# Optimization experiments

Measured on AMD Instinct MI355X. Metric: run time of the kernel, lower is better.

## Reference

```python
import jax, jax.numpy as jnp
import numpy as np

EPS = 1e-4
TAU = 0.1
GAMMA = 64.0
RADIUS = 1.0
N_HEADS = 4
N_SPLIT = 4


def _l2norm(x, axis=-1):
    return x / jnp.maximum(jnp.linalg.norm(x, axis=axis, keepdims=True), 1e-12)


def _pd2(a, b):
    # pairwise squared distances: (B,N,M)
    return (jnp.sum(a * a, -1)[:, :, None] + jnp.sum(b * b, -1)[:, None, :]
            - 2.0 * jnp.einsum('bnd,bmd->bnm', a, b))


def _sim_matrix(xyz, nf, radius, gamma):
    # radius-masked Gaussian feature affinity, zero diagonal
    N = xyz.shape[1]
    d2x = _pd2(xyz, xyz)
    d2f = _pd2(nf, nf)
    A = jnp.exp(-gamma * d2f / nf.shape[-1]) * (d2x < radius * radius).astype(nf.dtype)
    return A * (1.0 - jnp.eye(N, dtype=A.dtype))


def _norm_lap(A, eps):
    deg = A.sum(-1)
    dinv = jax.lax.rsqrt(deg + eps)
    na = A * dinv[:, :, None] * dinv[:, None, :]
    lap = jnp.eye(A.shape[1], dtype=A.dtype) - na
    return lap, na


def _mincut(X, na, W1, b1, W2, b2, tau):
    # one GCN layer + temperature softmax soft assignment; pooled = weighted mean
    h = jax.nn.relu(jnp.einsum('bnm,bmc->bnc', na, X) @ W1 + b1)
    s = jax.nn.softmax((h @ W2 + b2) / tau, axis=-1)  # (B,N,K)
    denom = s.sum(1)[:, :, None] + EPS                # (B,K,1)
    c_fea = jnp.einsum('bnk,bnc->bkc', s, X) / denom
    return c_fea, s


def _centers(xyz, s):
    denom = s.sum(1)[:, :, None] + EPS
    return jnp.einsum('bnk,bnd->bkd', s, xyz) / denom


def _assignment_loss(p_xyz, c_xyz, s):
    d2 = _pd2(p_xyz, c_xyz)
    return jnp.mean(jnp.sum(s * d2, -1))


def _welsch(p_xyz, c_xyz, sigma):
    d2min = jnp.min(_pd2(p_xyz, c_xyz), -1)
    return jnp.mean(1.0 - jnp.exp(-d2min / (2.0 * sigma * sigma)))


def _knn_affinity(xyz, k):
    N = xyz.shape[1]
    d2 = _pd2(xyz, xyz)
    eye = jnp.eye(N, dtype=d2.dtype)
    neg = -(d2 + 1e6 * eye)
    thresh = jax.lax.top_k(neg, k)[0][..., -1:]
    mask = (neg >= thresh).astype(d2.dtype)
    A = jnp.exp(-d2) * mask * (1.0 - eye)
    return jnp.maximum(A, jnp.swapaxes(A, 1, 2))


def _cut_loss(na, xyz, alpha):
    N = xyz.shape[1]
    lap = jnp.eye(N, dtype=na.dtype) - na
    quad = jnp.einsum('bnd,bnm,bmd->b', xyz, lap, xyz)
    return alpha * jnp.mean(quad / N)


def _cross_attn(gf, cf, Wq, Wk, Wv, Wo, n_heads):
    B, N, C = gf.shape
    M = cf.shape[1]
    dh = C // n_heads
    q = (gf @ Wq).reshape(B, N, n_heads, dh)
    k = (cf @ Wk).reshape(B, M, n_heads, dh)
    v = (cf @ Wv).reshape(B, M, n_heads, dh)
    scores = jnp.einsum('bnhd,bmhd->bhnm', q, k) / np.sqrt(dh).astype(np.float32)
    attn = jax.nn.softmax(scores, -1)
    out = jnp.einsum('bhnm,bmhd->bnhd', attn, v).reshape(B, N, C) @ Wo
    return out, attn.mean(1)


def setup_inputs() -> dict:
    key = jax.random.key(0)
    ks = jax.random.split(key, 20)
    B, N_sp, C, H, K = 2, 1024, 256, 128, 64
    Kg = K // N_SPLIT
    sc = 1.0 / np.sqrt(C)
    sh = 1.0 / np.sqrt(H)
    return {
        'g_fea': jax.random.normal(ks[0], (B, N_sp, C), jnp.float32),
        'g_xyz': jax.random.uniform(ks[1], (B, N_sp, 3), jnp.float32),
        'p_fea_0': jax.random.normal(ks[2], (B, 4096, C), jnp.float32),
        'p_xyz_0': jax.random.uniform(ks[3], (B, 4096, 3), jnp.float32),
        'p_fea_1': jax.random.normal(ks[4], (B, 2048, C), jnp.float32),
        'p_xyz_1': jax.random.uniform(ks[5], (B, 2048, 3), jnp.float32),
        'lW1': jax.random.normal(ks[6], (C, H), jnp.float32) * sc,
        'lb1': jnp.zeros((H,), jnp.float32),
        'lW2': jax.random.normal(ks[7], (H, K), jnp.float32) * sh,
        'lb2': jnp.zeros((K,), jnp.float32),
        'gW1': jax.random.normal(ks[8], (C, H), jnp.float32) * sc,
        'gb1': jnp.zeros((H,), jnp.float32),
        'gW2': jax.random.normal(ks[9], (H, Kg), jnp.float32) * sh,
        'gb2': jnp.zeros((Kg,), jnp.float32),
        'Wq': jax.random.normal(ks[10], (C, C), jnp.float32) * sc,
        'Wk': jax.random.normal(ks[11], (C, C), jnp.float32) * sc,
        'Wv': jax.random.normal(ks[12], (C, C), jnp.float32) * sc,
        'Wo': jax.random.normal(ks[13], (C, C), jnp.float32) * sc,
    }


def reference(g_fea, g_xyz, p_fea_0, p_xyz_0, p_fea_1, p_xyz_1,
              lW1, lb1, lW2, lb2, gW1, gb1, gW2, gb2, Wq, Wk, Wv, Wo):
    l_loss = jnp.zeros((), jnp.float32)
    cx_list, cf_list = [], []
    for p_xyz_i, p_fea_i in ((p_xyz_0, p_fea_0), (p_xyz_1, p_fea_1)):
        nf = _l2norm(p_fea_i)
        A = _sim_matrix(p_xyz_i, nf, RADIUS, GAMMA)
        na = _norm_lap(A, EPS)[1]
        c_fea_i, s_i = _mincut(p_fea_i, na, lW1, lb1, lW2, lb2, TAU)
        c_xyz_i = _centers(p_xyz_i, s_i)
        c2p = jnp.einsum('bnk,bkc->bnc', s_i, jax.lax.stop_gradient(c_fea_i))
        l_loss = l_loss + _assignment_loss(p_xyz_i, c_xyz_i, s_i)
        l_loss = l_loss + jnp.linalg.norm(_l2norm(c2p) - nf) + _welsch(p_xyz_i, c_xyz_i, 1.0)
        cx_list.append(c_xyz_i)
        cf_list.append(c_fea_i)
    c_xyz = jnp.concatenate(cx_list, 1)
    c_fea = jnp.concatenate(cf_list, 1)
    A_c = _knn_affinity(c_xyz, 2 * N_SPLIT)
    na_c = _norm_lap(A_c, EPS)[1]
    c_fea_g, gs = _mincut(c_fea, na_c, gW1, gb1, gW2, gb2, TAU)
    c_xyz_g = _centers(c_xyz, gs)
    cut_loss_c = _assignment_loss(c_xyz, c_xyz_g, gs)
    agg, G_t = _cross_attn(g_fea, c_fea_g, Wq, Wk, Wv, Wo, N_HEADS)
    A_g = _sim_matrix(g_xyz, _l2norm(g_fea), 4.0 * RADIUS, GAMMA)
    ass_loss = _cut_loss(_norm_lap(A_g, EPS)[1], g_xyz, 1e-4)
    g_loss = jnp.mean(jnp.sum(jnp.linalg.norm(_l2norm(agg) - _l2norm(g_fea), axis=-1), 1)) + ass_loss
    return agg, l_loss + cut_loss_c, g_loss
```

## Files before the change

kernel.cpp:

```cpp
#include <hip/hip_runtime.h>

#define EPSF 1e-4f

typedef __attribute__((ext_vector_type(8))) short bf16x8;
typedef __attribute__((ext_vector_type(4))) float f32x4;

__device__ __forceinline__ unsigned short f2bf(float f){
    unsigned int u = __float_as_uint(f);
    return (unsigned short)((u + 0x7FFF + ((u >> 16) & 1)) >> 16);
}
__device__ __forceinline__ float bf2f(unsigned short u){
    return __uint_as_float(((unsigned int)u) << 16);
}
__device__ __forceinline__ float waveSum(float v){
    #pragma unroll
    for (int o = 32; o; o >>= 1) v += __shfl_xor(v, o, 64);
    return v;
}
__device__ __forceinline__ float waveMin(float v){
    #pragma unroll
    for (int o = 32; o; o >>= 1) v = fminf(v, __shfl_xor(v, o, 64));
    return v;
}
__device__ __forceinline__ float waveMax(float v){
    #pragma unroll
    for (int o = 32; o; o >>= 1) v = fmaxf(v, __shfl_xor(v, o, 64));
    return v;
}
__device__ __forceinline__ float blockReduceSum(float v, float* red, int nthr){
    int t = threadIdx.x;
    red[t] = v; __syncthreads();
    for (int s = nthr >> 1; s > 0; s >>= 1){
        if (t < s) red[t] += red[t + s];
        __syncthreads();
    }
    float r = red[0]; __syncthreads();
    return r;
}

__global__ void l2norm_kernel(const float* __restrict__ x, unsigned short* __restrict__ outb, int rows){
    __shared__ float red[256];
    int row = blockIdx.x, t = threadIdx.x;
    float v = x[(long)row*256 + t];
    float s = blockReduceSum(v*v, red, 256);
    float nrm = fmaxf(sqrtf(s), 1e-12f);
    outb[(long)row*256 + t] = f2bf(v / nrm);
}

__global__ void cvt_bf16_kernel(const float* __restrict__ in, unsigned short* __restrict__ out, long n4){
    long i = (long)blockIdx.x*256 + threadIdx.x;
    if (i < n4){
        float4 v = ((const float4*)in)[i];
        unsigned int lo = f2bf(v.x) | ((unsigned int)f2bf(v.y) << 16);
        unsigned int hi = f2bf(v.z) | ((unsigned int)f2bf(v.w) << 16);
        uint2 u; u.x = lo; u.y = hi;
        ((uint2*)out)[i] = u;
    }
}

__global__ void tcvt_kernel(const float* __restrict__ W, unsigned short* __restrict__ WT,
                            int Rw, int Cw){
    __shared__ float tile[64][65];
    int r0 = blockIdx.x*64, c0 = blockIdx.y*64;
    int t = threadIdx.x;
    for (int idx = t; idx < 4096; idx += 256){
        int rr = idx >> 6, cc = idx & 63;
        tile[rr][cc] = (r0+rr < Rw && c0+cc < Cw) ? W[(long)(r0+rr)*Cw + c0+cc] : 0.f;
    }
    __syncthreads();
    for (int idx = t; idx < 4096; idx += 256){
        int cc = idx >> 6, rr = idx & 63;
        if (r0+rr < Rw && c0+cc < Cw)
            WT[(long)(c0+cc)*Rw + r0+rr] = f2bf(tile[rr][cc]);
    }
}

__global__ __launch_bounds__(256) void gram_mfma_kernel(const unsigned short* __restrict__ nf,
                                                        const float* __restrict__ xyz,
                                                        unsigned short* __restrict__ A,
                                                        float* __restrict__ deg,
                                                        int N, float r2, float scale){
    __shared__ short tA[128*32], tB[128*32];
    __shared__ float xa[384], xb[384];
    int tid = threadIdx.x;
    int n0 = blockIdx.y*128, m0 = blockIdx.x*128;
    for (int i = tid; i < 384; i += 256){ xa[i] = xyz[n0*3 + i]; xb[i] = xyz[m0*3 + i]; }
    int w = tid >> 6, l = tid & 63;
    int wy = w >> 1, wx = w & 1;
    int lg = l >> 4, lr = l & 15;
    int srow = tid >> 2, sc = tid & 3;
    f32x4 zero = {0.f, 0.f, 0.f, 0.f};
    f32x4 acc[4][4];
    #pragma unroll
    for (int i = 0; i < 4; ++i)
        #pragma unroll
        for (int j = 0; j < 4; ++j) acc[i][j] = zero;
    for (int kt = 0; kt < 256; kt += 32){
        __syncthreads();
        #pragma unroll
        for (int p = 0; p < 2; ++p){
            int row = srow + p*64;
            uint4 va = *(const uint4*)(nf + (long)(n0+row)*256 + kt + sc*8);
            uint4 vb = *(const uint4*)(nf + (long)(m0+row)*256 + kt + sc*8);
            *(uint4*)(tA + row*32 + sc*8) = va;
            *(uint4*)(tB + row*32 + sc*8) = vb;
        }
        __syncthreads();
        bf16x8 af[4], bfr[4];
        #pragma unroll
        for (int f = 0; f < 4; ++f){
            af[f]  = *(const bf16x8*)(tA + (wy*64 + f*16 + lr)*32 + lg*8);
            bfr[f] = *(const bf16x8*)(tB + (wx*64 + f*16 + lr)*32 + lg*8);
        }
        #pragma unroll
        for (int i = 0; i < 4; ++i)
            #pragma unroll
            for (int j = 0; j < 4; ++j)
                acc[i][j] = __builtin_amdgcn_mfma_f32_16x16x32_bf16(af[i], bfr[j], acc[i][j], 0, 0, 0);
    }
    #pragma unroll
    for (int fi = 0; fi < 4; ++fi){
        #pragma unroll
        for (int r = 0; r < 4; ++r){
            int n_ = wy*64 + fi*16 + lg*4 + r;
            int gn = n0 + n_;
            float rowacc = 0.f;
            #pragma unroll
            for (int fj = 0; fj < 4; ++fj){
                int m_ = wx*64 + fj*16 + lr;
                float dx = xa[n_*3+0]-xb[m_*3+0];
                float dy = xa[n_*3+1]-xb[m_*3+1];
                float dz = xa[n_*3+2]-xb[m_*3+2];
                float d2x = dx*dx + dy*dy + dz*dz;
                int gm = m0 + m_;
                float dot = acc[fi][fj][r];
                float val = (d2x < r2 && gn != gm) ? expf(scale*(2.f*dot - 2.f)) : 0.f;
                A[(long)gn*N + gm] = f2bf(val);
                rowacc += val;
            }
            rowacc += __shfl_xor(rowacc, 1, 64);
            rowacc += __shfl_xor(rowacc, 2, 64);
            rowacc += __shfl_xor(rowacc, 4, 64);
            rowacc += __shfl_xor(rowacc, 8, 64);
            if (lr == 0) atomicAdd(&deg[gn], rowacc);
        }
    }
}

__global__ __launch_bounds__(256) void transpose_scale_kernel(const float* __restrict__ fea,
                                                              const float* __restrict__ deg,
                                                              unsigned short* __restrict__ feaT,
                                                              unsigned short* __restrict__ xsT, int N){
    __shared__ float tile[64][65];
    __shared__ float dl[64];
    int m0 = blockIdx.x*64, c0 = blockIdx.y*64;
    int t = threadIdx.x;
    int lr = t >> 2, lc = (t & 3)*16;
    #pragma unroll
    for (int j = 0; j < 4; ++j){
        float4 v = *(const float4*)(fea + (long)(m0+lr)*256 + c0 + lc + j*4);
        tile[lr][lc+j*4+0] = v.x; tile[lr][lc+j*4+1] = v.y;
        tile[lr][lc+j*4+2] = v.z; tile[lr][lc+j*4+3] = v.w;
    }
    if (t < 64) dl[t] = rsqrtf(deg[m0+t] + EPSF);
    __syncthreads();
    unsigned short vr[16] __attribute__((aligned(16)));
    unsigned short vs[16] __attribute__((aligned(16)));
    #pragma unroll
    for (int j = 0; j < 16; ++j){
        float raw = tile[lc+j][lr];
        vr[j] = f2bf(raw);
        vs[j] = f2bf(raw * dl[lc+j]);
    }
    long off = (long)(c0+lr)*N + m0 + lc;
    *(uint4*)(feaT + off)     = *(uint4*)&vr[0];
    *(uint4*)(feaT + off + 8) = *(uint4*)&vr[8];
    *(uint4*)(xsT + off)      = *(uint4*)&vs[0];
    *(uint4*)(xsT + off + 8)  = *(uint4*)&vs[8];
}

__global__ __launch_bounds__(256) void ax_mfma_kernel(const unsigned short* __restrict__ A,
                                                      const unsigned short* __restrict__ xsT,
                                                      float* __restrict__ PY, int N, int split){
    __shared__ short tA[128*32], tB[128*32];
    int tid = threadIdx.x;
    int c0 = blockIdx.x*128, n0 = blockIdx.y*128;
    int chunk = blockIdx.z;
    int L = N/split, kbase = chunk*L, kend = kbase + L;
    int w = tid >> 6, l = tid & 63;
    int wy = w >> 1, wx = w & 1;
    int lg = l >> 4, lr = l & 15;
    int srow = tid >> 2, sc = tid & 3;
    f32x4 zero = {0.f, 0.f, 0.f, 0.f};
    f32x4 acc[4][4];
    #pragma unroll
    for (int i = 0; i < 4; ++i)
        #pragma unroll
        for (int j = 0; j < 4; ++j) acc[i][j] = zero;
    uint4 pva[2], pvb[2];
    #pragma unroll
    for (int p = 0; p < 2; ++p){
        int row = srow + p*64;
        pva[p] = *(const uint4*)(A   + (long)(n0+row)*N + kbase + sc*8);
        pvb[p] = *(const uint4*)(xsT + (long)(c0+row)*N + kbase + sc*8);
    }
    for (int kt = kbase; kt < kend; kt += 32){
        __syncthreads();
        #pragma unroll
        for (int p = 0; p < 2; ++p){
            int row = srow + p*64;
            *(uint4*)(tA + row*32 + sc*8) = pva[p];
            *(uint4*)(tB + row*32 + sc*8) = pvb[p];
        }
        __syncthreads();
        if (kt + 32 < kend){
            #pragma unroll
            for (int p = 0; p < 2; ++p){
                int row = srow + p*64;
                pva[p] = *(const uint4*)(A   + (long)(n0+row)*N + kt + 32 + sc*8);
                pvb[p] = *(const uint4*)(xsT + (long)(c0+row)*N + kt + 32 + sc*8);
            }
        }
        bf16x8 af[4], bfr[4];
        #pragma unroll
        for (int f = 0; f < 4; ++f){
            af[f]  = *(const bf16x8*)(tA + (wy*64 + f*16 + lr)*32 + lg*8);
            bfr[f] = *(const bf16x8*)(tB + (wx*64 + f*16 + lr)*32 + lg*8);
        }
        #pragma unroll
        for (int i = 0; i < 4; ++i)
            #pragma unroll
            for (int j = 0; j < 4; ++j)
                acc[i][j] = __builtin_amdgcn_mfma_f32_16x16x32_bf16(af[i], bfr[j], acc[i][j], 0, 0, 0);
    }
    float* out = PY + (long)chunk*N*256;
    #pragma unroll
    for (int fi = 0; fi < 4; ++fi){
        #pragma unroll
        for (int fj = 0; fj < 4; ++fj){
            #pragma unroll
            for (int r = 0; r < 4; ++r){
                int n_ = n0 + wy*64 + fi*16 + lg*4 + r;
                int c_ = c0 + wx*64 + fj*16 + lr;
                out[(long)n_*256 + c_] = acc[fi][fj][r];
            }
        }
    }
}

__global__ void combine_kernel(const float* __restrict__ PY, const float* __restrict__ deg,
                               unsigned short* __restrict__ Yb, int N, int split){
    long i = (long)blockIdx.x*256 + threadIdx.x;
    long e = i*8;
    float4 s0 = {0,0,0,0}, s1 = {0,0,0,0};
    for (int q = 0; q < split; ++q){
        const float4* p = (const float4*)(PY + (long)q*N*256 + e);
        float4 a = p[0], b = p[1];
        s0.x += a.x; s0.y += a.y; s0.z += a.z; s0.w += a.w;
        s1.x += b.x; s1.y += b.y; s1.z += b.z; s1.w += b.w;
    }
    float d = rsqrtf(deg[e >> 8] + EPSF);
    unsigned short vb[8] __attribute__((aligned(16)));
    vb[0] = f2bf(s0.x*d); vb[1] = f2bf(s0.y*d);
    vb[2] = f2bf(s0.z*d); vb[3] = f2bf(s0.w*d);
    vb[4] = f2bf(s1.x*d); vb[5] = f2bf(s1.y*d);
    vb[6] = f2bf(s1.z*d); vb[7] = f2bf(s1.w*d);
    *(uint4*)(Yb + e) = *(uint4*)vb;
}

__global__ __launch_bounds__(256) void gemm_XW_mfma_kernel(const unsigned short* __restrict__ X,
                                                           const unsigned short* __restrict__ WT,
                                                           const float* __restrict__ bias,
                                                           float* __restrict__ outF,
                                                           unsigned short* __restrict__ outB,
                                                           int R, int Ci, int Co, int relu){
    __shared__ short tA[128*32], tB[128*32];
    int tid = threadIdx.x;
    int c0 = blockIdx.x*128, r0 = blockIdx.y*128;
    int w = tid >> 6, l = tid & 63;
    int wy = w >> 1, wx = w & 1;
    int lg = l >> 4, lr = l & 15;
    int srow = tid >> 2, sc = tid & 3;
    f32x4 zero = {0.f, 0.f, 0.f, 0.f};
    f32x4 acc[4][4];
    #pragma unroll
    for (int i = 0; i < 4; ++i)
        #pragma unroll
        for (int j = 0; j < 4; ++j) acc[i][j] = zero;
    uint4 pva[2], pvb[2];
    #pragma unroll
    for (int p = 0; p < 2; ++p){
        int row = srow + p*64;
        int ar = r0 + row, br = c0 + row;
        pva[p] = (ar < R)  ? *(const uint4*)(X  + (long)ar*Ci + sc*8) : (uint4){0,0,0,0};
        pvb[p] = (br < Co) ? *(const uint4*)(WT + (long)br*Ci + sc*8) : (uint4){0,0,0,0};
    }
    for (int kt = 0; kt < Ci; kt += 32){
        __syncthreads();
        #pragma unroll
        for (int p = 0; p < 2; ++p){
            int row = srow + p*64;
            *(uint4*)(tA + row*32 + sc*8) = pva[p];
            *(uint4*)(tB + row*32 + sc*8) = pvb[p];
        }
        __syncthreads();
        if (kt + 32 < Ci){
            #pragma unroll
            for (int p = 0; p < 2; ++p){
                int row = srow + p*64;
                int ar = r0 + row, br = c0 + row;
                pva[p] = (ar < R)  ? *(const uint4*)(X  + (long)ar*Ci + kt + 32 + sc*8) : (uint4){0,0,0,0};
                pvb[p] = (br < Co) ? *(const uint4*)(WT + (long)br*Ci + kt + 32 + sc*8) : (uint4){0,0,0,0};
            }
        }
        bf16x8 af[4], bfr[4];
        #pragma unroll
        for (int f = 0; f < 4; ++f){
            af[f]  = *(const bf16x8*)(tA + (wy*64 + f*16 + lr)*32 + lg*8);
            bfr[f] = *(const bf16x8*)(tB + (wx*64 + f*16 + lr)*32 + lg*8);
        }
        #pragma unroll
        for (int i = 0; i < 4; ++i)
            #pragma unroll
            for (int j = 0; j < 4; ++j)
                acc[i][j] = __builtin_amdgcn_mfma_f32_16x16x32_bf16(af[i], bfr[j], acc[i][j], 0, 0, 0);
    }
    #pragma unroll
    for (int fi = 0; fi < 4; ++fi){
        #pragma unroll
        for (int fj = 0; fj < 4; ++fj){
            #pragma unroll
            for (int r = 0; r < 4; ++r){
                int rr = r0 + wy*64 + fi*16 + lg*4 + r;
                int cc = c0 + wx*64 + fj*16 + lr;
                if (rr < R && cc < Co){
                    float v = acc[fi][fj][r] + (bias ? bias[cc] : 0.f);
                    if (relu) v = fmaxf(v, 0.f);
                    if (outF) outF[(long)rr*Co + cc] = v;
                    if (outB) outB[(long)rr*Co + cc] = f2bf(v);
                }
            }
        }
    }
}

__global__ __launch_bounds__(256) void gemm_splitk_kernel(const float* __restrict__ X,
                                                          const float* __restrict__ W0,
                                                          const float* __restrict__ W1,
                                                          float* __restrict__ part,
                                                          int R, int Ci, int Co, int Ks){
    __shared__ float sa[32][65], sb[32][65];
    int tid = threadIdx.x, tx = tid & 15, ty = tid >> 4;
    int c0 = blockIdx.x * 64, r0 = blockIdx.y * 64;
    int z = blockIdx.z;
    const float* W = (z / Ks) ? W1 : W0;
    int kchunk = Ci / Ks, kst = (z % Ks) * kchunk;
    float acc[4][4] = {};
    for (int kt = kst; kt < kst + kchunk; kt += 32){
        #pragma unroll
        for (int p = 0; p < 8; ++p){
            int idx = p*256 + tid;
            int k = idx & 31, i = idx >> 5;
            int rr = r0 + i;
            sa[k][i] = (rr < R) ? X[(long)rr*Ci + kt + k] : 0.f;
            int j = idx & 63, kk = idx >> 6;
            int cc = c0 + j;
            sb[kk][j] = (cc < Co) ? W[(long)(kt+kk)*Co + cc] : 0.f;
        }
        __syncthreads();
        #pragma unroll
        for (int k = 0; k < 32; ++k){
            float a0=sa[k][ty*4+0],a1=sa[k][ty*4+1],a2=sa[k][ty*4+2],a3=sa[k][ty*4+3];
            float b0=sb[k][tx*4+0],b1=sb[k][tx*4+1],b2=sb[k][tx*4+2],b3=sb[k][tx*4+3];
            acc[0][0]+=a0*b0; acc[0][1]+=a0*b1; acc[0][2]+=a0*b2; acc[0][3]+=a0*b3;
            acc[1][0]+=a1*b0; acc[1][1]+=a1*b1; acc[1][2]+=a1*b2; acc[1][3]+=a1*b3;
            acc[2][0]+=a2*b0; acc[2][1]+=a2*b1; acc[2][2]+=a2*b2; acc[2][3]+=a2*b3;
            acc[3][0]+=a3*b0; acc[3][1]+=a3*b1; acc[3][2]+=a3*b2; acc[3][3]+=a3*b3;
        }
        __syncthreads();
    }
    float* outp = part + (long)z*R*Co;
    #pragma unroll
    for (int r = 0; r < 4; ++r){
        #pragma unroll
        for (int c = 0; c < 4; ++c){
            int rr = r0 + ty*4 + r, cc = c0 + tx*4 + c;
            if (rr < R && cc < Co) outp[(long)rr*Co + cc] = acc[r][c];
        }
    }
}

__global__ void combine_bias_kernel(const float* __restrict__ part, const float* __restrict__ bias,
                                    float* __restrict__ out, int R, int Co, int Ks, int relu){
    long i = (long)blockIdx.x*256 + threadIdx.x;
    if (i < (long)R*Co){
        long zs = (long)R*Co;
        float s = 0.f;
        for (int q = 0; q < Ks; ++q) s += part[q*zs + i];
        float v = s + (bias ? bias[i % Co] : 0.f);
        if (relu) v = fmaxf(v, 0.f);
        out[i] = v;
    }
}

__global__ __launch_bounds__(256) void softmaxT_kernel(float* __restrict__ s,
                                                       unsigned short* __restrict__ sT,
                                                       int sStride, float invtau){
    __shared__ unsigned short st[64][65];
    int blk = blockIdx.x, t = threadIdx.x, w = t >> 6, l = t & 63;
    #pragma unroll
    for (int i = 0; i < 16; ++i){
        int rloc = w + 4*i;
        long row = (long)blk*64 + rloc;
        float v = s[row*64 + l] * invtau;
        float mx = waveMax(v);
        float e = expf(v - mx);
        float sum = waveSum(e);
        float p = e / sum;
        s[row*64 + l] = p;
        st[l][rloc] = f2bf(p);
    }
    __syncthreads();
    int k = t >> 2, j = (t & 3)*16;
    unsigned short vbuf[16] __attribute__((aligned(16)));
    #pragma unroll
    for (int q = 0; q < 16; ++q) vbuf[q] = st[k][j+q];
    long off = (long)k*sStride + (long)blk*64 + j;
    *(uint4*)(sT + off)     = *(uint4*)&vbuf[0];
    *(uint4*)(sT + off + 8) = *(uint4*)&vbuf[8];
}

__global__ __launch_bounds__(256) void stx_mfma_kernel(const unsigned short* __restrict__ sT,
                                                       const unsigned short* __restrict__ feaT,
                                                       float* __restrict__ part,
                                                       int N, int split, int sStride){
    __shared__ short tA[64*32], tB[256*32];
    int tid = threadIdx.x;
    int z = blockIdx.x, b = z / split, chunk = z % split;
    int L = N / split, kst = chunk * L;
    const unsigned short* sTb = sT + (long)b*N;
    const unsigned short* fT  = feaT + (long)b*256*N;
    int w = tid >> 6, l = tid & 63;
    int lg = l >> 4, lr = l & 15;
    f32x4 zero = {0.f, 0.f, 0.f, 0.f};
    f32x4 acc[4][4];
    #pragma unroll
    for (int i = 0; i < 4; ++i)
        #pragma unroll
        for (int j = 0; j < 4; ++j) acc[i][j] = zero;
    int srow = tid >> 2, koff = (tid & 3)*8;
    for (int kt = kst; kt < kst + L; kt += 32){
        __syncthreads();
        *(uint4*)(tA + srow*32 + koff) = *(const uint4*)(sTb + (long)srow*sStride + kt + koff);
        #pragma unroll
        for (int p = 0; p < 4; ++p){
            int row = srow + p*64;
            *(uint4*)(tB + row*32 + koff) = *(const uint4*)(fT + (long)row*N + kt + koff);
        }
        __syncthreads();
        bf16x8 af[4], bfr[4];
        #pragma unroll
        for (int f = 0; f < 4; ++f){
            af[f]  = *(const bf16x8*)(tA + (f*16 + lr)*32 + lg*8);
            bfr[f] = *(const bf16x8*)(tB + (w*64 + f*16 + lr)*32 + lg*8);
        }
        #pragma unroll
        for (int i = 0; i < 4; ++i)
            #pragma unroll
            for (int j = 0; j < 4; ++j)
                acc[i][j] = __builtin_amdgcn_mfma_f32_16x16x32_bf16(af[i], bfr[j], acc[i][j], 0, 0, 0);
    }
    float* outp = part + (long)z*64*256;
    #pragma unroll
    for (int fi = 0; fi < 4; ++fi){
        #pragma unroll
        for (int fj = 0; fj < 4; ++fj){
            #pragma unroll
            for (int r = 0; r < 4; ++r){
                int kc = fi*16 + lg*4 + r;
                int cc = w*64 + fj*16 + lr;
                outp[(long)kc*256 + cc] = acc[fi][fj][r];
            }
        }
    }
}

__global__ void softmax_kernel(float* __restrict__ x, int Kc, float tau){
    int row = blockIdx.x, lane = threadIdx.x;
    bool act = lane < Kc;
    float v = act ? x[(long)row*Kc + lane] / tau : -1e30f;
    float mx = v;
    #pragma unroll
    for (int o = 32; o; o >>= 1) mx = fmaxf(mx, __shfl_xor(mx, o, 64));
    float e = act ? expf(v - mx) : 0.f;
    float s = e;
    #pragma unroll
    for (int o = 32; o; o >>= 1) s += __shfl_xor(s, o, 64);
    if (act) x[(long)row*Kc + lane] = e / s;
}

__global__ void cluster_xyz_kernel(const float* __restrict__ s, const float* __restrict__ xyz,
                                   float* __restrict__ outx, float* __restrict__ outd,
                                   int N, int Kc, int xBS, int dBS){
    __shared__ float red[256];
    int b = blockIdx.y, k = blockIdx.x, t = threadIdx.x;
    s   += (long)b*N*Kc;
    xyz += (long)b*N*3;
    float a0=0,a1=0,a2=0,ad=0;
    for (int n = t; n < N; n += 256){
        float sv = s[(long)n*Kc + k];
        ad += sv;
        a0 += sv*xyz[n*3+0]; a1 += sv*xyz[n*3+1]; a2 += sv*xyz[n*3+2];
    }
    a0 = blockReduceSum(a0, red, 256);
    a1 = blockReduceSum(a1, red, 256);
    a2 = blockReduceSum(a2, red, 256);
    ad = blockReduceSum(ad, red, 256);
    if (t == 0){
        outx[b*xBS + k*3+0] = a0;
        outx[b*xBS + k*3+1] = a1;
        outx[b*xBS + k*3+2] = a2;
        outd[b*dBS + k] = ad;
    }
}

__global__ __launch_bounds__(256) void gemm_sTX_kernel(const float* __restrict__ s,
                                                       const float* __restrict__ X,
                                                       float* __restrict__ part,
                                                       int N, int Kc, int split,
                                                       long sBS, long xBS){
    __shared__ float sa[32][65], sb[32][65];
    int tid = threadIdx.x, tx = tid & 15, ty = tid >> 4;
    int c0 = blockIdx.x * 64;
    int b = blockIdx.z / split, chunk = blockIdx.z % split;
    int L = N / split, nst = chunk * L;
    s += b*sBS; X += b*xBS;
    float* out = part + (long)blockIdx.z * Kc * 256;
    float acc[4][4] = {};
    for (int nt = nst; nt < nst + L; nt += 32){
        #pragma unroll
        for (int p = 0; p < 8; ++p){
            int idx = p*256 + tid;
            int i = idx & 63, k = idx >> 6;
            sa[k][i] = (i < Kc) ? s[(long)(nt+k)*Kc + i] : 0.f;
            int j = idx & 63, kk = idx >> 6;
            sb[kk][j] = X[(long)(nt+kk)*256 + c0 + j];
        }
// ... 197 lines not shown
                            const float* __restrict__ xyz, float* __restrict__ scal){
    __shared__ float part[4];
    int t = threadIdx.x, w = t >> 6, l = t & 63;
    int n = blockIdx.x*4 + w;
    float a0=0,a1=0,a2=0;
    #pragma unroll 4
    for (int i = 0; i < 16; ++i){
        int m = l + i*64;
        float wv = bf2f(A[(long)n*1024 + m])*rsqrtf(deg[m] + EPSF);
        a0 += wv*xyz[m*3+0]; a1 += wv*xyz[m*3+1]; a2 += wv*xyz[m*3+2];
    }
    a0 = waveSum(a0); a1 = waveSum(a1); a2 = waveSum(a2);
    if (l == 0){
        float x0 = xyz[n*3+0], x1 = xyz[n*3+1], x2 = xyz[n*3+2];
        float dn = rsqrtf(deg[n] + EPSF);
        part[w] = (x0*x0+x1*x1+x2*x2) - dn*(x0*a0+x1*a1+x2*a2);
    }
    __syncthreads();
    if (t == 0) atomicAdd(&scal[4*64 + (blockIdx.x & 63)], part[0]+part[1]+part[2]+part[3]);
}

__global__ void gloss_kernel(const float* __restrict__ agg, const float* __restrict__ gfea,
                             float* __restrict__ scal){
    __shared__ float part[4];
    int t = threadIdx.x, w = t >> 6, l = t & 63;
    long r = (long)blockIdx.x*4 + w;
    const float* a = agg + r*256;
    const float* g = gfea + r*256;
    float a0=a[l],a1=a[l+64],a2=a[l+128],a3=a[l+192];
    float g0=g[l],g1=g[l+64],g2=g[l+128],g3=g[l+192];
    float na2 = waveSum(a0*a0+a1*a1+a2*a2+a3*a3);
    float ng2 = waveSum(g0*g0+g1*g1+g2*g2+g3*g3);
    float ia = 1.f/fmaxf(sqrtf(na2), 1e-12f), ig = 1.f/fmaxf(sqrtf(ng2), 1e-12f);
    float e0=a0*ia-g0*ig, e1=a1*ia-g1*ig, e2=a2*ia-g2*ig, e3=a3*ia-g3*ig;
    float d2 = waveSum(e0*e0+e1*e1+e2*e2+e3*e3);
    if (l == 0) part[w] = sqrtf(d2);
    __syncthreads();
    if (t == 0) atomicAdd(&scal[3*64 + (blockIdx.x & 63)], part[0]+part[1]+part[2]+part[3]);
}

__global__ void finalize_kernel(const float* __restrict__ scal, float* __restrict__ out){
    int t = threadIdx.x;
    float s[5];
    #pragma unroll
    for (int q = 0; q < 5; ++q){
        float v = scal[q*64 + t];
        #pragma unroll
        for (int o = 32; o; o >>= 1) v += __shfl_xor(v, o, 64);
        s[q] = v;
    }
    if (t == 0){
        out[524288] = s[0] + sqrtf(s[1]) + sqrtf(s[2]);
        out[524289] = s[3]*0.5f + 1e-4f*s[4]/2048.0f;
    }
}

extern "C" void kernel_launch(void* const* d_in, const int* in_sizes, int n_in,
                              void* d_out, int out_size, void* d_ws, size_t ws_size,
                              hipStream_t stream){
    const float* g_fea   = (const float*)d_in[0];
    const float* g_xyz   = (const float*)d_in[1];
    const float* p_fea_0 = (const float*)d_in[2];
    const float* p_xyz_0 = (const float*)d_in[3];
    const float* p_fea_1 = (const float*)d_in[4];
    const float* p_xyz_1 = (const float*)d_in[5];
    const float* lW1 = (const float*)d_in[6];
    const float* lb1 = (const float*)d_in[7];
    const float* lW2 = (const float*)d_in[8];
    const float* lb2 = (const float*)d_in[9];
    const float* gW1 = (const float*)d_in[10];
    const float* gb1 = (const float*)d_in[11];
    const float* gW2 = (const float*)d_in[12];
    const float* gb2 = (const float*)d_in[13];
    const float* Wq = (const float*)d_in[14];
    const float* Wk = (const float*)d_in[15];
    const float* Wv = (const float*)d_in[16];
    const float* Wo = (const float*)d_in[17];
    float* out = (float*)d_out;
    float* ws_f = (float*)d_ws;

    constexpr long O_SCALS = 0;
    constexpr long O_DEG   = 512;
    constexpr long O_CFEA  = 16384;
    constexpr long O_CXYZ  = O_CFEA + 65536;
    constexpr long O_DEN   = O_CXYZ + 768;
    constexpr long O_CFG   = O_DEN  + 256;
    constexpr long O_CXG   = O_CFG  + 8192;
    constexpr long O_DENG  = O_CXG  + 96;
    constexpr long O_PART  = O_DENG + 64;
    constexpr long O_NFB   = O_PART + 524288;
    constexpr long O_XST   = O_NFB  + 1048576;
    constexpr long O_FEAT  = O_XST  + 1048576;
    constexpr long O_YB    = O_FEAT + 1048576;
    constexpr long O_HB    = O_YB   + 1048576;
    constexpr long O_S     = O_HB   + 524288;
    constexpr long O_ST    = O_S    + 524288;
    constexpr long O_PY    = O_ST   + 262144;
    constexpr long O_A     = O_PY   + 8388608;
    constexpr long O_Q     = O_A    + 8388608;
    constexpr long O_GFB   = O_Q    + 524288;
    constexpr long O_AOB   = O_GFB  + 262144;
    constexpr long O_KK    = O_AOB  + 262144;
    constexpr long O_VV    = O_KK   + 8192;
    constexpr long O_NAC   = O_VV   + 8192;
    constexpr long O_Y2    = O_NAC  + 32768;
    constexpr long O_H2    = O_Y2   + 65536;
    constexpr long O_LG2   = O_H2   + 32768;
    constexpr long O_W1T   = O_LG2  + 4096;
    constexpr long O_W2T   = O_W1T  + 16384;
    constexpr long O_WQT   = O_W2T  + 4096;
    constexpr long O_WOT   = O_WQT  + 32768;

    hipMemsetAsync(ws_f + O_SCALS, 0, (512 + 14336)*sizeof(float), stream);

    unsigned short* nfb  = (unsigned short*)(ws_f + O_NFB);
    unsigned short* xsT  = (unsigned short*)(ws_f + O_XST);
    unsigned short* feaT = (unsigned short*)(ws_f + O_FEAT);
    unsigned short* Ybb  = (unsigned short*)(ws_f + O_YB);
    unsigned short* Hb   = (unsigned short*)(ws_f + O_HB);
    unsigned short* sTb  = (unsigned short*)(ws_f + O_ST);
    unsigned short* A    = (unsigned short*)(ws_f + O_A);
    unsigned short* gfb  = (unsigned short*)(ws_f + O_GFB);
    unsigned short* aob  = (unsigned short*)(ws_f + O_AOB);
    unsigned short* lW1T = (unsigned short*)(ws_f + O_W1T);
    unsigned short* lW2T = (unsigned short*)(ws_f + O_W2T);
    unsigned short* WqT  = (unsigned short*)(ws_f + O_WQT);
    unsigned short* WoT  = (unsigned short*)(ws_f + O_WOT);
    float* sb   = ws_f + O_S;
    float* degA = ws_f + O_DEG;
    float* PY   = ws_f + O_PY;
    float* part = ws_f + O_PART;
    float* Qf   = ws_f + O_Q;

    tcvt_kernel<<<dim3(4, 2), 256, 0, stream>>>(lW1, lW1T, 256, 128);
    tcvt_kernel<<<dim3(2, 1), 256, 0, stream>>>(lW2, lW2T, 128, 64);
    tcvt_kernel<<<dim3(4, 4), 256, 0, stream>>>(Wq, WqT, 256, 256);
    tcvt_kernel<<<dim3(4, 4), 256, 0, stream>>>(Wo, WoT, 256, 256);
    cvt_bf16_kernel<<<512, 256, 0, stream>>>(g_fea, gfb, 131072);

    struct Lvl { const float* fea; const float* xyz; int N; int k0; int ndsSlot; long degBase; };
    Lvl lv[2] = {{p_fea_0, p_xyz_0, 4096, 0, 1, 0}, {p_fea_1, p_xyz_1, 2048, 64, 2, 8192}};

    for (int L = 0; L < 2; ++L){
        int N = lv[L].N;
        const float* fea = lv[L].fea;
        const float* xyz = lv[L].xyz;
        l2norm_kernel<<<2*N, 256, 0, stream>>>(fea, nfb, 2*N);
        for (int b = 0; b < 2; ++b){
            float* degb = degA + lv[L].degBase + (long)b*N;
            gram_mfma_kernel<<<dim3(N/128, N/128), 256, 0, stream>>>(nfb + (long)b*N*256,
                                                                     xyz + (long)b*N*3, A, degb,
                                                                     N, 1.0f, 0.25f);
            transpose_scale_kernel<<<dim3(N/64, 4), 256, 0, stream>>>(fea + (long)b*N*256, degb,
                                                                      feaT + (long)b*256*N,
                                                                      xsT + (long)b*256*N, N);
            ax_mfma_kernel<<<dim3(2, N/128, 8), 256, 0, stream>>>(A, xsT + (long)b*256*N, PY, N, 8);
            combine_kernel<<<N/8, 256, 0, stream>>>(PY, degb, Ybb + (long)b*N*256, N, 8);
        }
        gemm_XW_mfma_kernel<<<dim3(1, 2*N/128), 256, 0, stream>>>(Ybb, lW1T, lb1, nullptr, Hb,
                                                                  2*N, 256, 128, 1);
        gemm_XW_mfma_kernel<<<dim3(1, 2*N/128), 256, 0, stream>>>(Hb, lW2T, lb2, sb, nullptr,
                                                                  2*N, 128, 64, 0);
        softmaxT_kernel<<<2*N/64, 256, 0, stream>>>(sb, sTb, 2*N, 10.0f);
        cluster_xyz_kernel<<<dim3(64, 2), 256, 0, stream>>>(sb, xyz, ws_f + O_CXYZ + lv[L].k0*3,
                                                            ws_f + O_DEN + lv[L].k0, N, 64, 384, 128);
        stx_mfma_kernel<<<32, 256, 0, stream>>>(sTb, feaT, part, N, 16, 2*N);
        divide_sum_kernel<<<dim3(64, 2), 256, 0, stream>>>(part, ws_f + O_DEN + lv[L].k0,
                                                           ws_f + O_CFEA + lv[L].k0*256,
                                                           ws_f + O_CXYZ + lv[L].k0*3,
                                                           64, 16, 128*256, 384, 128);
        level_loss_kernel<<<dim3(N/4, 2), 256, 0, stream>>>(sb, xyz, ws_f + O_CXYZ + lv[L].k0*3,
                                                            ws_f + O_CFEA + lv[L].k0*256, nfb,
                                                            ws_f + O_SCALS, N, 1.0f/(2.0f*N), lv[L].ndsSlot);
    }

    knn_nac_kernel<<<2, 128, 0, stream>>>(ws_f + O_CXYZ, ws_f + O_NAC);
    bmm_small_kernel<<<dim3(128, 2), 256, 0, stream>>>(ws_f + O_NAC, ws_f + O_CFEA, ws_f + O_Y2);
    gemm_splitk_kernel<<<dim3(2, 4, 4), 256, 0, stream>>>(ws_f + O_Y2, gW1, nullptr, part,
                                                          256, 256, 128, 4);
    combine_bias_kernel<<<128, 256, 0, stream>>>(part, gb1, ws_f + O_H2, 256, 128, 4, 1);
    gemm_splitk_kernel<<<dim3(1, 4, 4), 256, 0, stream>>>(ws_f + O_H2, gW2, nullptr, part,
                                                          256, 128, 16, 4);
    combine_bias_kernel<<<16, 256, 0, stream>>>(part, gb2, ws_f + O_LG2, 256, 16, 4, 0);
    softmax_kernel<<<256, 64, 0, stream>>>(ws_f + O_LG2, 16, 0.1f);
    cluster_xyz_kernel<<<dim3(16, 2), 256, 0, stream>>>(ws_f + O_LG2, ws_f + O_CXYZ,
                                                        ws_f + O_CXG, ws_f + O_DENG, 128, 16, 48, 16);
    gemm_sTX_kernel<<<dim3(4, 1, 8), 256, 0, stream>>>(ws_f + O_LG2, ws_f + O_CFEA, part,
                                                       128, 16, 4, 128L*16, 128L*256);
    divide_sum_kernel<<<dim3(16, 2), 256, 0, stream>>>(part, ws_f + O_DENG, ws_f + O_CFG,
                                                       ws_f + O_CXG, 16, 4, 16*256, 48, 16);
    cutc_kernel<<<2, 128, 0, stream>>>(ws_f + O_LG2, ws_f + O_CXYZ, ws_f + O_CXG,
                                       ws_f + O_SCALS, 1.0f/256.0f);

    gemm_XW_mfma_kernel<<<dim3(2, 16), 256, 0, stream>>>(gfb, WqT, nullptr, Qf, nullptr,
                                                         2048, 256, 256, 0);
    gemm_splitk_kernel<<<dim3(4, 1, 16), 256, 0, stream>>>(ws_f + O_CFG, Wk, Wv, part,
                                                           32, 256, 256, 8);
    combine_bias_kernel<<<32, 256, 0, stream>>>(part, nullptr, ws_f + O_KK, 32, 256, 8, 0);
    combine_bias_kernel<<<32, 256, 0, stream>>>(part + 8L*32*256, nullptr, ws_f + O_VV, 32, 256, 8, 0);
    attn_kernel<<<dim3(1024, 2), 256, 0, stream>>>(Qf, ws_f + O_KK, ws_f + O_VV, aob);
    gemm_XW_mfma_kernel<<<dim3(2, 16), 256, 0, stream>>>(aob, WoT, nullptr, out, nullptr,
                                                         2048, 256, 256, 0);

    l2norm_kernel<<<2048, 256, 0, stream>>>(g_fea, nfb, 2048);
    for (int b = 0; b < 2; ++b){
        float* degb = degA + 12288 + (long)b*1024;
        gram_mfma_kernel<<<dim3(8, 8), 256, 0, stream>>>(nfb + (long)b*1024*256, g_xyz + (long)b*1024*3,
                                                         A, degb, 1024, 16.0f, 0.25f);
        quad_kernel<<<256, 256, 0, stream>>>(A, degb, g_xyz + (long)b*1024*3, ws_f + O_SCALS);
    }

    gloss_kernel<<<512, 256, 0, stream>>>(out, g_fea, ws_f + O_SCALS);
    finalize_kernel<<<1, 64, 0, stream>>>(ws_f + O_SCALS, out);
}
```

Measured before the change: 770.0 us.

## Pad LDS tiles, shrink ax tile width, batch both levels' MLP GEMMs

Measured after the change: 756.8 us. About the same (-1.7%).

```diff
diff --git a/kernel.cpp b/kernel.cpp
--- a/kernel.cpp
+++ b/kernel.cpp
@@ -80,7 +80,7 @@
                                                         unsigned short* __restrict__ A,
                                                         float* __restrict__ deg,
                                                         int N, float r2, float scale){
-    __shared__ short tA[128*32], tB[128*32];
+    __shared__ short tA[128*40], tB[128*40];
     __shared__ float xa[384], xb[384];
     int tid = threadIdx.x;
     int n0 = blockIdx.y*128, m0 = blockIdx.x*128;
@@ -102,15 +102,15 @@
             int row = srow + p*64;
             uint4 va = *(const uint4*)(nf + (long)(n0+row)*256 + kt + sc*8);
             uint4 vb = *(const uint4*)(nf + (long)(m0+row)*256 + kt + sc*8);
-            *(uint4*)(tA + row*32 + sc*8) = va;
-            *(uint4*)(tB + row*32 + sc*8) = vb;
+            *(uint4*)(tA + row*40 + sc*8) = va;
+            *(uint4*)(tB + row*40 + sc*8) = vb;
         }
         __syncthreads();
         bf16x8 af[4], bfr[4];
         #pragma unroll
         for (int f = 0; f < 4; ++f){
-            af[f]  = *(const bf16x8*)(tA + (wy*64 + f*16 + lr)*32 + lg*8);
-            bfr[f] = *(const bf16x8*)(tB + (wx*64 + f*16 + lr)*32 + lg*8);
+            af[f]  = *(const bf16x8*)(tA + (wy*64 + f*16 + lr)*40 + lg*8);
+            bfr[f] = *(const bf16x8*)(tB + (wx*64 + f*16 + lr)*40 + lg*8);
         }
         #pragma unroll
         for (int i = 0; i < 4; ++i)
@@ -182,9 +182,9 @@
 __global__ __launch_bounds__(256) void ax_mfma_kernel(const unsigned short* __restrict__ A,
                                                       const unsigned short* __restrict__ xsT,
                                                       float* __restrict__ PY, int N, int split){
-    __shared__ short tA[128*32], tB[128*32];
+    __shared__ short tA[128*40], tB[64*40];
     int tid = threadIdx.x;
-    int c0 = blockIdx.x*128, n0 = blockIdx.y*128;
+    int c0 = blockIdx.x*64, n0 = blockIdx.y*128;
     int chunk = blockIdx.z;
     int L = N/split, kbase = chunk*L, kend = kbase + L;
     int w = tid >> 6, l = tid & 63;
@@ -192,56 +192,51 @@
     int lg = l >> 4, lr = l & 15;
     int srow = tid >> 2, sc = tid & 3;
     f32x4 zero = {0.f, 0.f, 0.f, 0.f};
-    f32x4 acc[4][4];
+    f32x4 acc[4][2];
     #pragma unroll
     for (int i = 0; i < 4; ++i)
         #pragma unroll
-        for (int j = 0; j < 4; ++j) acc[i][j] = zero;
-    uint4 pva[2], pvb[2];
-    #pragma unroll
-    for (int p = 0; p < 2; ++p){
-        int row = srow + p*64;
-        pva[p] = *(const uint4*)(A   + (long)(n0+row)*N + kbase + sc*8);
-        pvb[p] = *(const uint4*)(xsT + (long)(c0+row)*N + kbase + sc*8);
-    }
+        for (int j = 0; j < 2; ++j) acc[i][j] = zero;
+    uint4 pva[2], pvb;
+    #pragma unroll
+    for (int p = 0; p < 2; ++p)
+        pva[p] = *(const uint4*)(A + (long)(n0+srow+p*64)*N + kbase + sc*8);
+    pvb = *(const uint4*)(xsT + (long)(c0+srow)*N + kbase + sc*8);
     for (int kt = kbase; kt < kend; kt += 32){
         __syncthreads();
         #pragma unroll
-        for (int p = 0; p < 2; ++p){
-            int row = srow + p*64;
-            *(uint4*)(tA + row*32 + sc*8) = pva[p];
-            *(uint4*)(tB + row*32 + sc*8) = pvb[p];
-        }
+        for (int p = 0; p < 2; ++p)
+            *(uint4*)(tA + (srow+p*64)*40 + sc*8) = pva[p];
+        *(uint4*)(tB + srow*40 + sc*8) = pvb;
         __syncthreads();
         if (kt + 32 < kend){
             #pragma unroll
-            for (int p = 0; p < 2; ++p){
-                int row = srow + p*64;
-                pva[p] = *(const uint4*)(A   + (long)(n0+row)*N + kt + 32 + sc*8);
-                pvb[p] = *(const uint4*)(xsT + (long)(c0+row)*N + kt + 32 + sc*8);
-            }
-        }
-        bf16x8 af[4], bfr[4];
-        #pragma unroll
-        for (int f = 0; f < 4; ++f){
-            af[f]  = *(const bf16x8*)(tA + (wy*64 + f*16 + lr)*32 + lg*8);
-            bfr[f] = *(const bf16x8*)(tB + (wx*64 + f*16 + lr)*32 + lg*8);
-        }
+            for (int p = 0; p < 2; ++p)
+                pva[p] = *(const uint4*)(A + (long)(n0+srow+p*64)*N + kt + 32 + sc*8);
+            pvb = *(const uint4*)(xsT + (long)(c0+srow)*N + kt + 32 + sc*8);
+        }
+        bf16x8 af[4], bfr[2];
+        #pragma unroll
+        for (int f = 0; f < 4; ++f)
+            af[f] = *(const bf16x8*)(tA + (wy*64 + f*16 + lr)*40 + lg*8);
+        #pragma unroll
+        for (int f = 0; f < 2; ++f)
+            bfr[f] = *(const bf16x8*)(tB + (wx*32 + f*16 + lr)*40 + lg*8);
         #pragma unroll
         for (int i = 0; i < 4; ++i)
             #pragma unroll
-            for (int j = 0; j < 4; ++j)
+            for (int j = 0; j < 2; ++j)
                 acc[i][j] = __builtin_amdgcn_mfma_f32_16x16x32_bf16(af[i], bfr[j], acc[i][j], 0, 0, 0);
     }
     float* out = PY + (long)chunk*N*256;
     #pragma unroll
     for (int fi = 0; fi < 4; ++fi){
         #pragma unroll
-        for (int fj = 0; fj < 4; ++fj){
+        for (int fj = 0; fj < 2; ++fj){
             #pragma unroll
             for (int r = 0; r < 4; ++r){
                 int n_ = n0 + wy*64 + fi*16 + lg*4 + r;
-                int c_ = c0 + wx*64 + fj*16 + lr;
+                int c_ = c0 + wx*32 + fj*16 + lr;
                 out[(long)n_*256 + c_] = acc[fi][fj][r];
             }
         }
@@ -274,7 +269,7 @@
                                                            float* __restrict__ outF,
                                                            unsigned short* __restrict__ outB,
                                                            int R, int Ci, int Co, int relu){
-    __shared__ short tA[128*32], tB[128*32];
+    __shared__ short tA[128*40], tB[128*40];
     int tid = threadIdx.x;
     int c0 = blockIdx.x*128, r0 = blockIdx.y*128;
     int w = tid >> 6, l = tid & 63;
@@ -300,8 +295,8 @@
         #pragma unroll
         for (int p = 0; p < 2; ++p){
             int row = srow + p*64;
-            *(uint4*)(tA + row*32 + sc*8) = pva[p];
-            *(uint4*)(tB + row*32 + sc*8) = pvb[p];
+            *(uint4*)(tA + row*40 + sc*8) = pva[p];
+            *(uint4*)(tB + row*40 + sc*8) = pvb[p];
         }
         __syncthreads();
         if (kt + 32 < Ci){
@@ -316,8 +311,8 @@
         bf16x8 af[4], bfr[4];
         #pragma unroll
         for (int f = 0; f < 4; ++f){
-            af[f]  = *(const bf16x8*)(tA + (wy*64 + f*16 + lr)*32 + lg*8);
-            bfr[f] = *(const bf16x8*)(tB + (wx*64 + f*16 + lr)*32 + lg*8);
+            af[f]  = *(const bf16x8*)(tA + (wy*64 + f*16 + lr)*40 + lg*8);
+            bfr[f] = *(const bf16x8*)(tB + (wx*64 + f*16 + lr)*40 + lg*8);
         }
         #pragma unroll
         for (int i = 0; i < 4; ++i)
@@ -434,7 +429,7 @@
                                                        const unsigned short* __restrict__ feaT,
                                                        float* __restrict__ part,
                                                        int N, int split, int sStride){
-    __shared__ short tA[64*32], tB[256*32];
+    __shared__ short tA[64*40], tB[256*40];
     int tid = threadIdx.x;
     int z = blockIdx.x, b = z / split, chunk = z % split;
     int L = N / split, kst = chunk * L;
@@ -451,18 +446,18 @@
     int srow = tid >> 2, koff = (tid & 3)*8;
     for (int kt = kst; kt < kst + L; kt += 32){
         __syncthreads();
-        *(uint4*)(tA + srow*32 + koff) = *(const uint4*)(sTb + (long)srow*sStride + kt + koff);
+        *(uint4*)(tA + srow*40 + koff) = *(const uint4*)(sTb + (long)srow*sStride + kt + koff);
         #pragma unroll
         for (int p = 0; p < 4; ++p){
             int row = srow + p*64;
-            *(uint4*)(tB + row*32 + koff) = *(const uint4*)(fT + (long)row*N + kt + koff);
+            *(uint4*)(tB + row*40 + koff) = *(const uint4*)(fT + (long)row*N + kt + koff);
         }
         __syncthreads();
         bf16x8 af[4], bfr[4];
         #pragma unroll
         for (int f = 0; f < 4; ++f){
-            af[f]  = *(const bf16x8*)(tA + (f*16 + lr)*32 + lg*8);
-            bfr[f] = *(const bf16x8*)(tB + (w*64 + f*16 + lr)*32 + lg*8);
+            af[f]  = *(const bf16x8*)(tA + (f*16 + lr)*40 + lg*8);
+            bfr[f] = *(const bf16x8*)(tB + (w*64 + f*16 + lr)*40 + lg*8);
         }
         #pragma unroll
         for (int i = 0; i < 4; ++i)
@@ -826,20 +821,19 @@
     constexpr long O_SCALS = 0;
     constexpr long O_DEG   = 512;
     constexpr long O_CFEA  = 16384;
-    constexpr long O_CXYZ  = O_CFEA + 65536;
-    constexpr long O_DEN   = O_CXYZ + 768;
-    constexpr long O_CFG   = O_DEN  + 256;
-    constexpr long O_CXG   = O_CFG  + 8192;
-    constexpr long O_DENG  = O_CXG  + 96;
-    constexpr long O_PART  = O_DENG + 64;
-    constexpr long O_NFB   = O_PART + 524288;
-    constexpr long O_XST   = O_NFB  + 1048576;
+    constexpr long O_CXYZ  = 81920;
+    constexpr long O_DEN   = 82688;
+    constexpr long O_CFG   = 82944;
+    constexpr long O_CXG   = 91136;
+    constexpr long O_DENG  = 91232;
+    constexpr long O_NFB   = 91296;
+    constexpr long O_XST   = O_NFB  + 1572864;
     constexpr long O_FEAT  = O_XST  + 1048576;
-    constexpr long O_YB    = O_FEAT + 1048576;
-    constexpr long O_HB    = O_YB   + 1048576;
-    constexpr long O_S     = O_HB   + 524288;
-    constexpr long O_ST    = O_S    + 524288;
-    constexpr long O_PY    = O_ST   + 262144;
+    constexpr long O_YB    = O_FEAT + 1572864;
+    constexpr long O_HB    = O_YB   + 1572864;
+    constexpr long O_S     = O_HB   + 786432;
+    constexpr long O_ST    = O_S    + 786432;
+    constexpr long O_PY    = O_ST   + 393216;
     constexpr long O_A     = O_PY   + 8388608;
     constexpr long O_Q     = O_A    + 8388608;
     constexpr long O_GFB   = O_Q    + 524288;
@@ -873,7 +867,6 @@
     float* sb   = ws_f + O_S;
     float* degA = ws_f + O_DEG;
     float* PY   = ws_f + O_PY;
-    float* part = ws_f + O_PART;
     float* Qf   = ws_f + O_Q;
 
     tcvt_kernel<<<dim3(4, 2), 256, 0, stream>>>(lW1, lW1T, 256, 128);
@@ -882,66 +875,80 @@
     tcvt_kernel<<<dim3(4, 4), 256, 0, stream>>>(Wo, WoT, 256, 256);
     cvt_bf16_kernel<<<512, 256, 0, stream>>>(g_fea, gfb, 131072);
 
-    struct Lvl { const float* fea; const float* xyz; int N; int k0; int ndsSlot; long degBase; };
-    Lvl lv[2] = {{p_fea_0, p_xyz_0, 4096, 0, 1, 0}, {p_fea_1, p_xyz_1, 2048, 64, 2, 8192}};
+    struct Lvl { const float* fea; const float* xyz; int N; int k0; int ndsSlot; long degBase;
+                 long rowOff; long featOff; };
+    Lvl lv[2] = {{p_fea_0, p_xyz_0, 4096, 0, 1, 0, 0, 0},
+                 {p_fea_1, p_xyz_1, 2048, 64, 2, 8192, 8192, 2097152}};
 
     for (int L = 0; L < 2; ++L){
         int N = lv[L].N;
         const float* fea = lv[L].fea;
         const float* xyz = lv[L].xyz;
-        l2norm_kernel<<<2*N, 256, 0, stream>>>(fea, nfb, 2*N);
+        unsigned short* nfbL  = nfb + lv[L].rowOff*256;
+        unsigned short* feaTL = feaT + lv[L].featOff;
+        l2norm_kernel<<<2*N, 256, 0, stream>>>(fea, nfbL, 2*N);
         for (int b = 0; b < 2; ++b){
             float* degb = degA + lv[L].degBase + (long)b*N;
-            gram_mfma_kernel<<<dim3(N/128, N/128), 256, 0, stream>>>(nfb + (long)b*N*256,
+            gram_mfma_kernel<<<dim3(N/128, N/128), 256, 0, stream>>>(nfbL + (long)b*N*256,
                                                                      xyz + (long)b*N*3, A, degb,
                                                                      N, 1.0f, 0.25f);
             transpose_scale_kernel<<<dim3(N/64, 4), 256, 0, stream>>>(fea + (long)b*N*256, degb,
-                                                                      feaT + (long)b*256*N,
+                                                                      feaTL + (long)b*256*N,
                                                                       xsT + (long)b*256*N, N);
-            ax_mfma_kernel<<<dim3(2, N/128, 8), 256, 0, stream>>>(A, xsT + (long)b*256*N, PY, N, 8);
-            combine_kernel<<<N/8, 256, 0, stream>>>(PY, degb, Ybb + (long)b*N*256, N, 8);
-        }
-        gemm_XW_mfma_kernel<<<dim3(1, 2*N/128), 256, 0, stream>>>(Ybb, lW1T, lb1, nullptr, Hb,
-                                                                  2*N, 256, 128, 1);
-        gemm_XW_mfma_kernel<<<dim3(1, 2*N/128), 256, 0, stream>>>(Hb, lW2T, lb2, sb, nullptr,
-                                                                  2*N, 128, 64, 0);
-        softmaxT_kernel<<<2*N/64, 256, 0, stream>>>(sb, sTb, 2*N, 10.0f);
-        cluster_xyz_kernel<<<dim3(64, 2), 256, 0, stream>>>(sb, xyz, ws_f + O_CXYZ + lv[L].k0*3,
+            ax_mfma_kernel<<<dim3(4, N/128, 8), 256, 0, stream>>>(A, xsT + (long)b*256*N, PY, N, 8);
+            combine_kernel<<<N/8, 256, 0, stream>>>(PY, degb,
+                                                    Ybb + (lv[L].rowOff + (long)b*N)*256, N, 8);
+        }
+    }
+
+    gemm_XW_mfma_kernel<<<dim3(1, 96), 256, 0, stream>>>(Ybb, lW1T, lb1, nullptr, Hb,
+                                                         12288, 256, 128, 1);
+    gemm_XW_mfma_kernel<<<dim3(1, 96), 256, 0, stream>>>(Hb, lW2T, lb2, sb, nullptr,
+                                                         12288, 128, 64, 0);
+    softmaxT_kernel<<<192, 256, 0, stream>>>(sb, sTb, 12288, 10.0f);
+
+    for (int L = 0; L < 2; ++L){
+        int N = lv[L].N;
+        const float* xyz = lv[L].xyz;
+        float* sL = sb + lv[L].rowOff*64;
+        cluster_xyz_kernel<<<dim3(64, 2), 256, 0, stream>>>(sL, xyz, ws_f + O_CXYZ + lv[L].k0*3,
                                                             ws_f + O_DEN + lv[L].k0, N, 64, 384, 128);
-        stx_mfma_kernel<<<32, 256, 0, stream>>>(sTb, feaT, part, N, 16, 2*N);
-        divide_sum_kernel<<<dim3(64, 2), 256, 0, stream>>>(part, ws_f + O_DEN + lv[L].k0,
+        stx_mfma_kernel<<<32, 256, 0, stream>>>(sTb + lv[L].rowOff, feaT + lv[L].featOff,
+                                                PY, N, 16, 12288);
+        divide_sum_kernel<<<dim3(64, 2), 256, 0, stream>>>(PY, ws_f + O_DEN + lv[L].k0,
                                                            ws_f + O_CFEA + lv[L].k0*256,
                                                            ws_f + O_CXYZ + lv[L].k0*3,
                                                            64, 16, 128*256, 384, 128);
-        level_loss_kernel<<<dim3(N/4, 2), 256, 0, stream>>>(sb, xyz, ws_f + O_CXYZ + lv[L].k0*3,
-                                                            ws_f + O_CFEA + lv[L].k0*256, nfb,
+        level_loss_kernel<<<dim3(N/4, 2), 256, 0, stream>>>(sL, xyz, ws_f + O_CXYZ + lv[L].k0*3,
+                                                            ws_f + O_CFEA + lv[L].k0*256,
+                                                            nfb + lv[L].rowOff*256,
                                                             ws_f + O_SCALS, N, 1.0f/(2.0f*N), lv[L].ndsSlot);
     }
 
     knn_nac_kernel<<<2, 128, 0, stream>>>(ws_f + O_CXYZ, ws_f + O_NAC);
     bmm_small_kernel<<<dim3(128, 2), 256, 0, stream>>>(ws_f + O_NAC, ws_f + O_CFEA, ws_f + O_Y2);
-    gemm_splitk_kernel<<<dim3(2, 4, 4), 256, 0, stream>>>(ws_f + O_Y2, gW1, nullptr, part,
+    gemm_splitk_kernel<<<dim3(2, 4, 4), 256, 0, stream>>>(ws_f + O_Y2, gW1, nullptr, PY,
                                                           256, 256, 128, 4);
-    combine_bias_kernel<<<128, 256, 0, stream>>>(part, gb1, ws_f + O_H2, 256, 128, 4, 1);
-    gemm_splitk_kernel<<<dim3(1, 4, 4), 256, 0, stream>>>(ws_f + O_H2, gW2, nullptr, part,
+    combine_bias_kernel<<<128, 256, 0, stream>>>(PY, gb1, ws_f + O_H2, 256, 128, 4, 1);
+    gemm_splitk_kernel<<<dim3(1, 4, 4), 256, 0, stream>>>(ws_f + O_H2, gW2, nullptr, PY,
                                                           256, 128, 16, 4);
-    combine_bias_kernel<<<16, 256, 0, stream>>>(part, gb2, ws_f + O_LG2, 256, 16, 4, 0);
+    combine_bias_kernel<<<16, 256, 0, stream>>>(PY, gb2, ws_f + O_LG2, 256, 16, 4, 0);
     softmax_kernel<<<256, 64, 0, stream>>>(ws_f + O_LG2, 16, 0.1f);
     cluster_xyz_kernel<<<dim3(16, 2), 256, 0, stream>>>(ws_f + O_LG2, ws_f + O_CXYZ,
                                                         ws_f + O_CXG, ws_f + O_DENG, 128, 16, 48, 16);
-    gemm_sTX_kernel<<<dim3(4, 1, 8), 256, 0, stream>>>(ws_f + O_LG2, ws_f + O_CFEA, part,
+    gemm_sTX_kernel<<<dim3(4, 1, 8), 256, 0, stream>>>(ws_f + O_LG2, ws_f + O_CFEA, PY,
                                                        128, 16, 4, 128L*16, 128L*256);
-    divide_sum_kernel<<<dim3(16, 2), 256, 0, stream>>>(part, ws_f + O_DENG, ws_f + O_CFG,
+    divide_sum_kernel<<<dim3(16, 2), 256, 0, stream>>>(PY, ws_f + O_DENG, ws_f + O_CFG,
                                                        ws_f + O_CXG, 16, 4, 16*256, 48, 16);
     cutc_kernel<<<2, 128, 0, stream>>>(ws_f + O_LG2, ws_f + O_CXYZ, ws_f + O_CXG,
                                        ws_f + O_SCALS, 1.0f/256.0f);
 
     gemm_XW_mfma_kernel<<<dim3(2, 16), 256, 0, stream>>>(gfb, WqT, nullptr, Qf, nullptr,
                                                          2048, 256, 256, 0);
-    gemm_splitk_kernel<<<dim3(4, 1, 16), 256, 0, stream>>>(ws_f + O_CFG, Wk, Wv, part,
+    gemm_splitk_kernel<<<dim3(4, 1, 16), 256, 0, stream>>>(ws_f + O_CFG, Wk, Wv, PY,
                                                            32, 256, 256, 8);
-    combine_bias_kernel<<<32, 256, 0, stream>>>(part, nullptr, ws_f + O_KK, 32, 256, 8, 0);
-    combine_bias_kernel<<<32, 256, 0, stream>>>(part + 8L*32*256, nullptr, ws_f + O_VV, 32, 256, 8, 0);
+    combine_bias_kernel<<<32, 256, 0, stream>>>(PY, nullptr, ws_f + O_KK, 32, 256, 8, 0);
+    combine_bias_kernel<<<32, 256, 0, stream>>>(PY + 8L*32*256, nullptr, ws_f + O_VV, 32, 256, 8, 0);
     attn_kernel<<<dim3(1024, 2), 256, 0, stream>>>(Qf, ws_f + O_KK, ws_f + O_VV, aob);
     gemm_XW_mfma_kernel<<<dim3(2, 16), 256, 0, stream>>>(aob, WoT, nullptr, out, nullptr,
                                                          2048, 256, 256, 0);
```
